# Performance work log

Measured on AMD Instinct MI355X. Metric: run time of the kernel, lower is better.

The kernel has to match this reference:

```python
import jax, jax.numpy as jnp
import numpy as np

B, S, H = 2, 8192, 1024
NUM_HEADS = 16
HEAD_DIM = H // NUM_HEADS
KERNEL = 7
DILATION = 1
SCALE = 1.0 / np.sqrt(HEAD_DIM)


def setup_inputs() -> dict:
    key = jax.random.key(0)
    ks = jax.random.split(key, 9)
    init = 0.02
    return {
        "hidden_states": jax.random.normal(ks[0], (B, S, H), dtype=jnp.float32),
        "w_q": jax.random.normal(ks[1], (H, H), dtype=jnp.float32) * init,
        "b_q": jnp.zeros((H,), dtype=jnp.float32),
        "w_k": jax.random.normal(ks[2], (H, H), dtype=jnp.float32) * init,
        "b_k": jnp.zeros((H,), dtype=jnp.float32),
        "w_v": jax.random.normal(ks[3], (H, H), dtype=jnp.float32) * init,
        "b_v": jnp.zeros((H,), dtype=jnp.float32),
        "w_o": jax.random.normal(ks[4], (H, H), dtype=jnp.float32) * init,
        "b_o": jnp.zeros((H,), dtype=jnp.float32),
    }


def reference(hidden_states, w_q, b_q, w_k, b_k, w_v, b_v, w_o, b_o):
    b, s, h = hidden_states.shape
    # QKV projections (weights stored [in, out])
    q = hidden_states @ w_q + b_q
    k = hidden_states @ w_k + b_k
    v = hidden_states @ w_v + b_v
    # [B, nH, S, hd]
    q = q.reshape(b, s, NUM_HEADS, HEAD_DIM).transpose(0, 2, 1, 3)
    k = k.reshape(b, s, NUM_HEADS, HEAD_DIM).transpose(0, 2, 1, 3)
    v = v.reshape(b, s, NUM_HEADS, HEAD_DIM).transpose(0, 2, 1, 3)

    # Neighborhood window indices: for query i, keys at i + (j - K//2)*dilation
    offsets = (jnp.arange(KERNEL) - KERNEL // 2) * DILATION  # [K]
    idx = jnp.arange(s)[:, None] + offsets[None, :]          # [S, K]
    valid = (idx >= 0) & (idx < s)                           # [S, K]
    idx_c = jnp.clip(idx, 0, s - 1)

    k_win = k[:, :, idx_c, :]  # [B, nH, S, K, hd]
    v_win = v[:, :, idx_c, :]  # [B, nH, S, K, hd]

    scores = jnp.einsum('bhsd,bhskd->bhsk', q, k_win) * SCALE
    scores = jnp.where(valid[None, None], scores, -jnp.inf)
    attn = jax.nn.softmax(scores, axis=-1)                   # [B, nH, S, K]
    out = jnp.einsum('bhsk,bhskd->bhsd', attn, v_win)        # [B, nH, S, hd]

    out = out.transpose(0, 2, 1, 3).reshape(b, s, h)
    return out @ w_o + b_o
```

## Files before the change

### kernel.cpp

```cpp
#include <hip/hip_runtime.h>


typedef __bf16 bf16x8 __attribute__((ext_vector_type(8)));
typedef float f32x4 __attribute__((ext_vector_type(4)));
typedef int int4v __attribute__((ext_vector_type(4)));
typedef __attribute__((address_space(1))) void as1_void;
typedef __attribute__((address_space(3))) void as3_void;

__device__ __forceinline__ float bf2f(unsigned short u) {
    union { unsigned int u; float f; } c;
    c.u = ((unsigned int)u) << 16;
    return c.f;
}
__device__ __forceinline__ unsigned short f2bf(float f) {
    union { float f; unsigned int u; } c;
    c.f = f;
    unsigned int u = c.u;
    u += 0x7fffu + ((u >> 16) & 1u);
    return (unsigned short)(u >> 16);
}

__global__ __launch_bounds__(256) void cast_kernel(
    const float* __restrict__ in, unsigned short* __restrict__ out, int n4) {
    int i = blockIdx.x * 256 + threadIdx.x;
    if (i < n4) {
        float4 v = ((const float4*)in)[i];
        ushort4 o;
        o.x = f2bf(v.x); o.y = f2bf(v.y); o.z = f2bf(v.z); o.w = f2bf(v.w);
        ((ushort4*)out)[i] = o;
    }
}

__global__ __launch_bounds__(256) void transpose_cast(
    const float* __restrict__ W, unsigned short* __restrict__ Wt) {
    __shared__ unsigned short tile[32][33];
    const int c0 = blockIdx.x * 32;
    const int r0 = blockIdx.y * 32;
    const int tx = threadIdx.x;
    const int ty = threadIdx.y;
#pragma unroll
    for (int i = 0; i < 32; i += 8)
        tile[ty + i][tx] = f2bf(W[(size_t)(r0 + ty + i) * 1024 + c0 + tx]);
    __syncthreads();
#pragma unroll
    for (int i = 0; i < 32; i += 8)
        Wt[(size_t)(c0 + ty + i) * 1024 + r0 + tx] = tile[tx][ty + i];
}

__global__ __launch_bounds__(256) void concat_bias(
    const float* __restrict__ a, const float* __restrict__ b,
    const float* __restrict__ c, float* __restrict__ o) {
    int i = blockIdx.x * 256 + threadIdx.x;
    if (i < 3072)
        o[i] = (i < 1024) ? a[i] : ((i < 2048) ? b[i - 1024] : c[i - 2048]);
}

template <int MODE>
__global__ __launch_bounds__(256) void gemm_bt(
    const unsigned short* __restrict__ A, const unsigned short* __restrict__ Bt,
    const float* __restrict__ bias, float* __restrict__ Cf,
    unsigned short* __restrict__ Cb, unsigned short* __restrict__ Vt,
    int N, int K) {
    __shared__ unsigned short smem[16384];
    const int tid = threadIdx.x;
    const int lane = tid & 63;
    const int wave = tid >> 6;
    const int bm = blockIdx.y * 128;
    const int bn = blockIdx.x * 128;
    const int wm = (wave >> 1) * 64;
    const int wn = (wave & 1) * 64;
    const int quad = lane >> 4;
    const int mr = lane & 15;

    const unsigned short* gA[4];
    const unsigned short* gB[4];
    char* lA[4];
    char* lB[4];
#pragma unroll
    for (int k = 0; k < 4; ++k) {
        const int q = (k * 4 + wave) * 64 + lane;
        const int row = q >> 3;
        const int c8 = (q & 7) ^ (row & 7);
        gA[k] = A + (size_t)(bm + row) * K + c8 * 8;
        gB[k] = Bt + (size_t)(bn + row) * K + c8 * 8;
        lA[k] = (char*)smem + (size_t)(k * 4 + wave) * 1024;
        lB[k] = (char*)smem + 16384 + (size_t)(k * 4 + wave) * 1024;
    }

    f32x4 acc[4][4] = {};

    for (int kt = 0; kt < K; kt += 64) {
#pragma unroll
        for (int k = 0; k < 4; ++k) {
            __builtin_amdgcn_global_load_lds((as1_void*)gA[k], (as3_void*)lA[k], 16, 0, 0);
            __builtin_amdgcn_global_load_lds((as1_void*)gB[k], (as3_void*)lB[k], 16, 0, 0);
            gA[k] += 64; gB[k] += 64;
        }
        __syncthreads();

#pragma unroll
        for (int kk = 0; kk < 2; ++kk) {
            bf16x8 af[4], bfr[4];
#pragma unroll
            for (int i = 0; i < 4; ++i) {
                const int R = wm + i * 16 + mr;
                const int c8 = (kk * 4 + quad) ^ (mr & 7);
                af[i] = *(const bf16x8*)(smem + R * 64 + c8 * 8);
            }
#pragma unroll
            for (int j = 0; j < 4; ++j) {
                const int R = wn + j * 16 + mr;
                const int c8 = (kk * 4 + quad) ^ (mr & 7);
                bfr[j] = *(const bf16x8*)(smem + 8192 + R * 64 + c8 * 8);
            }
#pragma unroll
            for (int i = 0; i < 4; ++i)
#pragma unroll
                for (int j = 0; j < 4; ++j)
                    acc[i][j] = __builtin_amdgcn_mfma_f32_16x16x32_bf16(
                        af[i], bfr[j], acc[i][j], 0, 0, 0);
        }
        __syncthreads();
    }

    if (MODE == 0 || bn < 2048) {
#pragma unroll
        for (int j = 0; j < 4; ++j) {
            const int gcol = bn + wn + j * 16 + mr;
            const float bv = bias[gcol];
#pragma unroll
            for (int i = 0; i < 4; ++i) {
                const int gr = bm + wm + i * 16 + quad * 4;
#pragma unroll
                for (int r = 0; r < 4; ++r) {
                    const float v = acc[i][j][r] + bv;
                    if (MODE == 0) Cf[(size_t)(gr + r) * N + gcol] = v;
                    else           Cb[(size_t)(gr + r) * 2048 + gcol] = f2bf(v);
                }
            }
        }
    } else {
        unsigned short* ep = smem + wave * 2048;
        const int bb = (bm + wm) >> 13;
        const int ssb = (bm + wm) & 8191;
        const int lr = ((lane & 15) == lane ? 0 : 0);
#pragma unroll
        for (int j = 0; j < 4; ++j) {
            const int gcol = bn + wn + j * 16 + mr;
            const float bv = bias[gcol];
#pragma unroll
            for (int i = 0; i < 4; ++i)
#pragma unroll
                for (int r = 0; r < 4; ++r)
                    ep[mr * 68 + i * 16 + quad * 4 + r] = f2bf(acc[i][j][r] + bv);
            const size_t vrow0 = (size_t)(bb * 1024 + (bn - 2048) + wn + j * 16);
#pragma unroll
            for (int p = 0; p < 4; ++p) {
                const int dr = (p * 64 + lane) >> 4;
                const int ch = lane & 15;
                uint2 val = *(const uint2*)(ep + dr * 68 + ch * 4);
                *(uint2*)(Vt + (vrow0 + dr) * 8192 + ssb + ch * 4) = val;
            }
        }
        (void)lr;
    }
}

__global__ __launch_bounds__(256) void attn_mfma(
    const unsigned short* __restrict__ QK, const unsigned short* __restrict__ Vt,
    unsigned short* __restrict__ out) {
    __shared__ unsigned short sP[4][64 * 104];
    const int tid = threadIdx.x;
    const int lane = tid & 63;
    const int wave = tid >> 6;
    const int quad = lane >> 4;
    const int cc = lane & 15;
    const int w = blockIdx.x * 4 + wave;
    const int b = w >> 11;
    const int h = (w >> 7) & 15;
    const int st = w & 127;
    const int s0 = st << 6;
    const int win0 = s0 - 8;
    const size_t tokBase = (size_t)b * 8192;
    unsigned short* P = sP[wave];

    {
        int4v z = {0, 0, 0, 0};
#pragma unroll
        for (int i = 0; i < 13; ++i)
            *(int4v*)(P + i * 512 + lane * 8) = z;
    }

    f32x4 accS[4][5] = {};
#pragma unroll
    for (int kc = 0; kc < 2; ++kc) {
        bf16x8 qf[4], kf[5];
#pragma unroll
        for (int mt = 0; mt < 4; ++mt)
            qf[mt] = *(const bf16x8*)(QK + (tokBase + s0 + mt * 16 + cc) * 2048
                                      + h * 64 + kc * 32 + quad * 8);
#pragma unroll
        for (int nt = 0; nt < 5; ++nt) {
            int row = win0 + nt * 16 + cc;
            row = row < 0 ? 0 : (row > 8191 ? 8191 : row);
            kf[nt] = *(const bf16x8*)(QK + (tokBase + row) * 2048
                                      + 1024 + h * 64 + kc * 32 + quad * 8);
        }
#pragma unroll
        for (int mt = 0; mt < 4; ++mt)
#pragma unroll
            for (int nt = 0; nt < 5; ++nt)
                accS[mt][nt] = __builtin_amdgcn_mfma_f32_16x16x32_bf16(
                    qf[mt], kf[nt], accS[mt][nt], 0, 0, 0);
    }

    const float NEG = -__builtin_inff();
#pragma unroll
    for (int mt = 0; mt < 4; ++mt) {
#pragma unroll
        for (int r = 0; r < 4; ++r) {
            const int mrow = mt * 16 + quad * 4 + r;
            float v[5];
#pragma unroll
            for (int nt = 0; nt < 5; ++nt) {
                const int k = nt * 16 + cc;
                const int rel = k - mrow;
                const int sidx = win0 + k;
                const bool ok = (rel >= 5) & (rel <= 11) & (sidx >= 0) & (sidx < 8192);
                v[nt] = ok ? accS[mt][nt][r] * 0.125f : NEG;
            }
            float mx = v[0];
#pragma unroll
            for (int nt = 1; nt < 5; ++nt) mx = fmaxf(mx, v[nt]);
#pragma unroll
            for (int off = 8; off >= 1; off >>= 1) mx = fmaxf(mx, __shfl_xor(mx, off));
            float p[5], sum = 0.f;
#pragma unroll
            for (int nt = 0; nt < 5; ++nt) {
                p[nt] = __builtin_amdgcn_exp2f((v[nt] - mx) * 1.44269504f);
                sum += p[nt];
            }
#pragma unroll
            for (int off = 8; off >= 1; off >>= 1) sum += __shfl_xor(sum, off);
            const float inv = __builtin_amdgcn_rcpf(sum);
#pragma unroll
            for (int nt = 0; nt < 5; ++nt)
                P[mrow * 104 + nt * 16 + cc] = f2bf(p[nt] * inv);
        }
    }

    f32x4 accO[4][4] = {};
#pragma unroll
    for (int kc = 0; kc < 3; ++kc) {
        bf16x8 pf[4], vf[4];
#pragma unroll
        for (int mt = 0; mt < 4; ++mt)
            pf[mt] = *(const bf16x8*)(P + (mt * 16 + cc) * 104 + kc * 32 + quad * 8);
        {
            int pos = win0 + kc * 32 + quad * 8;
            pos = pos < 0 ? 0 : (pos > 8184 ? 8184 : pos);
#pragma unroll
            for (int nt = 0; nt < 4; ++nt)
                vf[nt] = *(const bf16x8*)(Vt + ((size_t)(b * 16 + h) * 64 + nt * 16 + cc) * 8192 + pos);
        }
#pragma unroll
        for (int mt = 0; mt < 4; ++mt)
#pragma unroll
            for (int nt = 0; nt < 4; ++nt)
                accO[mt][nt] = __builtin_amdgcn_mfma_f32_16x16x32_bf16(
                    pf[mt], vf[nt], accO[mt][nt], 0, 0, 0);
    }

#pragma unroll
    for (int mt = 0; mt < 4; ++mt)
#pragma unroll
        for (int nt = 0; nt < 4; ++nt)
#pragma unroll
            for (int r = 0; r < 4; ++r)
                P[(mt * 16 + quad * 4 + r) * 72 + nt * 16 + cc] = f2bf(accO[mt][nt][r]);

#pragma unroll
    for (int pass = 0; pass < 8; ++pass) {
        const int row = pass * 8 + (lane >> 3);
        const int ch = lane & 7;
        int4v vv = *(const int4v*)(P + row * 72 + ch * 8);
        *(int4v*)(out + (tokBase + s0 + row) * 1024 + h * 64 + ch * 8) = vv;
    }
}

extern "C" void kernel_launch(void* const* d_in, const int* in_sizes, int n_in,
                              void* d_out, int out_size, void* d_ws, size_t ws_size,
                              hipStream_t stream) {
    (void)in_sizes; (void)n_in; (void)out_size; (void)ws_size;
    const float* X  = (const float*)d_in[0];
    const float* wq = (const float*)d_in[1];
    const float* bq = (const float*)d_in[2];
    const float* wk = (const float*)d_in[3];
    const float* bk = (const float*)d_in[4];
    const float* wv = (const float*)d_in[5];
    const float* bv = (const float*)d_in[6];
    const float* wo = (const float*)d_in[7];
    const float* bo = (const float*)d_in[8];
    float* out = (float*)d_out;

    char* ws = (char*)d_ws;
    unsigned short* Xb    = (unsigned short*)(ws);
    unsigned short* WtQKV = (unsigned short*)(ws + 33554432);
    unsigned short* WtO   = (unsigned short*)(ws + 39845888);
    unsigned short* QK    = (unsigned short*)(ws + 41943040);
    unsigned short* Vt    = (unsigned short*)(ws + 109051904);
    unsigned short* AttnO = (unsigned short*)(ws + 142606336);
    float*          biasQ = (float*)(ws + 176160768);

    cast_kernel<<<16384, 256, 0, stream>>>(X, Xb, 4194304);

    dim3 tb(32, 8), tg(32, 32);
    transpose_cast<<<tg, tb, 0, stream>>>(wq, WtQKV);
    transpose_cast<<<tg, tb, 0, stream>>>(wk, WtQKV + 1024 * 1024);
    transpose_cast<<<tg, tb, 0, stream>>>(wv, WtQKV + 2 * 1024 * 1024);
    transpose_cast<<<tg, tb, 0, stream>>>(wo, WtO);
    concat_bias<<<12, 256, 0, stream>>>(bq, bk, bv, biasQ);

    gemm_bt<1><<<dim3(24, 128), 256, 0, stream>>>(Xb, WtQKV, biasQ, nullptr, QK, Vt, 3072, 1024);

    attn_mfma<<<1024, 256, 0, stream>>>(QK, Vt, AttnO);

    gemm_bt<0><<<dim3(8, 128), 256, 0, stream>>>(AttnO, WtO, bo, out, nullptr, nullptr, 1024, 1024);
}
```

Before: 353.9 us.

## Stage GEMM epilogues through LDS, swizzle tile order, merge weight transposes

The GEMM epilogues now stage each wave's output tile in shared memory and write rows back with 16-byte vector stores, replacing scattered scalar stores for both the fp32 output and the bf16 Q/K outputs. Block indices are remapped so groups of 16 row-tiles sweep across the columns together, which is meant to improve L2 reuse of the A and B operands. The four weight transpose-cast launches are merged into one launch over a z dimension, cutting launch overhead. The extra LDS round trip adds a little shared-memory traffic and instruction work in the epilogue.

```diff
diff --git a/kernel.cpp b/kernel.cpp
--- a/kernel.cpp
+++ b/kernel.cpp
@@ -31,13 +31,18 @@
     }
 }
 
-__global__ __launch_bounds__(256) void transpose_cast(
-    const float* __restrict__ W, unsigned short* __restrict__ Wt) {
+__global__ __launch_bounds__(256) void transpose_cast4(
+    const float* __restrict__ w0, const float* __restrict__ w1,
+    const float* __restrict__ w2, const float* __restrict__ w3,
+    unsigned short* __restrict__ t0, unsigned short* __restrict__ t3) {
     __shared__ unsigned short tile[32][33];
+    const int z = blockIdx.z;
+    const float* W = (z == 0) ? w0 : (z == 1) ? w1 : (z == 2) ? w2 : w3;
+    unsigned short* Wt = (z == 3) ? t3 : t0 + (size_t)z * 1048576;
     const int c0 = blockIdx.x * 32;
     const int r0 = blockIdx.y * 32;
-    const int tx = threadIdx.x;
-    const int ty = threadIdx.y;
+    const int tx = threadIdx.x & 31;
+    const int ty = threadIdx.x >> 5;
 #pragma unroll
     for (int i = 0; i < 32; i += 8)
         tile[ty + i][tx] = f2bf(W[(size_t)(r0 + ty + i) * 1024 + c0 + tx]);
@@ -56,7 +61,7 @@
 }
 
 template <int MODE>
-__global__ __launch_bounds__(256) void gemm_bt(
+__device__ __forceinline__ void gemm_body(
     const unsigned short* __restrict__ A, const unsigned short* __restrict__ Bt,
     const float* __restrict__ bias, float* __restrict__ Cf,
     unsigned short* __restrict__ Cb, unsigned short* __restrict__ Vt,
@@ -65,8 +70,15 @@
     const int tid = threadIdx.x;
     const int lane = tid & 63;
     const int wave = tid >> 6;
-    const int bm = blockIdx.y * 128;
-    const int bn = blockIdx.x * 128;
+
+    const int nbx = gridDim.x;
+    const int n = blockIdx.y * nbx + blockIdx.x;
+    const int per = nbx * 16;
+    const int g = n / per;
+    const int rm = n - g * per;
+    const int bm = (g * 16 + (rm & 15)) * 128;
+    const int bn = (rm >> 4) * 128;
+
     const int wm = (wave >> 1) * 64;
     const int wn = (wave & 1) * 64;
     const int quad = lane >> 4;
@@ -123,27 +135,48 @@
         __syncthreads();
     }
 
-    if (MODE == 0 || bn < 2048) {
+    if (MODE == 0) {
+        float* epf = (float*)smem + wave * 2048;
 #pragma unroll
         for (int j = 0; j < 4; ++j) {
-            const int gcol = bn + wn + j * 16 + mr;
-            const float bv = bias[gcol];
-#pragma unroll
-            for (int i = 0; i < 4; ++i) {
-                const int gr = bm + wm + i * 16 + quad * 4;
-#pragma unroll
-                for (int r = 0; r < 4; ++r) {
-                    const float v = acc[i][j][r] + bv;
-                    if (MODE == 0) Cf[(size_t)(gr + r) * N + gcol] = v;
-                    else           Cb[(size_t)(gr + r) * 2048 + gcol] = f2bf(v);
-                }
+            const int gcol0 = bn + wn + j * 16;
+            const float bv = bias[gcol0 + mr];
+#pragma unroll
+            for (int i = 0; i < 4; ++i)
+#pragma unroll
+                for (int r = 0; r < 4; ++r)
+                    epf[(i * 16 + quad * 4 + r) * 20 + mr] = acc[i][j][r] + bv;
+#pragma unroll
+            for (int p = 0; p < 4; ++p) {
+                const int dr = p * 16 + (lane >> 2);
+                const int ch = lane & 3;
+                f32x4 v = *(const f32x4*)(epf + dr * 20 + ch * 4);
+                *(f32x4*)(Cf + (size_t)(bm + wm + dr) * N + gcol0 + ch * 4) = v;
+            }
+        }
+    } else if (bn < 2048) {
+        unsigned short* epb = smem + wave * 4096;
+#pragma unroll
+        for (int j = 0; j < 4; ++j) {
+            const int gcol0 = bn + wn + j * 16;
+            const float bv = bias[gcol0 + mr];
+#pragma unroll
+            for (int i = 0; i < 4; ++i)
+#pragma unroll
+                for (int r = 0; r < 4; ++r)
+                    epb[(i * 16 + quad * 4 + r) * 20 + mr] = f2bf(acc[i][j][r] + bv);
+#pragma unroll
+            for (int p = 0; p < 2; ++p) {
+                const int dr = p * 32 + (lane >> 1);
+                const int ch = lane & 1;
+                int4v v = *(const int4v*)(epb + dr * 20 + ch * 8);
+                *(int4v*)(Cb + (size_t)(bm + wm + dr) * 2048 + gcol0 + ch * 8) = v;
             }
         }
     } else {
-        unsigned short* ep = smem + wave * 2048;
+        unsigned short* ep = smem + wave * 4096;
         const int bb = (bm + wm) >> 13;
         const int ssb = (bm + wm) & 8191;
-        const int lr = ((lane & 15) == lane ? 0 : 0);
 #pragma unroll
         for (int j = 0; j < 4; ++j) {
             const int gcol = bn + wn + j * 16 + mr;
@@ -162,8 +195,20 @@
                 *(uint2*)(Vt + (vrow0 + dr) * 8192 + ssb + ch * 4) = val;
             }
         }
-        (void)lr;
-    }
+    }
+}
+
+__global__ __launch_bounds__(256) void gemm_qkv(
+    const unsigned short* __restrict__ A, const unsigned short* __restrict__ Bt,
+    const float* __restrict__ bias, unsigned short* __restrict__ Cb,
+    unsigned short* __restrict__ Vt, int N, int K) {
+    gemm_body<1>(A, Bt, bias, nullptr, Cb, Vt, N, K);
+}
+
+__global__ __launch_bounds__(256) void gemm_out(
+    const unsigned short* __restrict__ A, const unsigned short* __restrict__ Bt,
+    const float* __restrict__ bias, float* __restrict__ Cf, int N, int K) {
+    gemm_body<0>(A, Bt, bias, Cf, nullptr, nullptr, N, K);
 }
 
 __global__ __launch_bounds__(256) void attn_mfma(
@@ -313,17 +358,12 @@
     float*          biasQ = (float*)(ws + 176160768);
 
     cast_kernel<<<16384, 256, 0, stream>>>(X, Xb, 4194304);
-
-    dim3 tb(32, 8), tg(32, 32);
-    transpose_cast<<<tg, tb, 0, stream>>>(wq, WtQKV);
-    transpose_cast<<<tg, tb, 0, stream>>>(wk, WtQKV + 1024 * 1024);
-    transpose_cast<<<tg, tb, 0, stream>>>(wv, WtQKV + 2 * 1024 * 1024);
-    transpose_cast<<<tg, tb, 0, stream>>>(wo, WtO);
+    transpose_cast4<<<dim3(32, 32, 4), 256, 0, stream>>>(wq, wk, wv, wo, WtQKV, WtO);
     concat_bias<<<12, 256, 0, stream>>>(bq, bk, bv, biasQ);
 
-    gemm_bt<1><<<dim3(24, 128), 256, 0, stream>>>(Xb, WtQKV, biasQ, nullptr, QK, Vt, 3072, 1024);
+    gemm_qkv<<<dim3(24, 128), 256, 0, stream>>>(Xb, WtQKV, biasQ, QK, Vt, 3072, 1024);
 
     attn_mfma<<<1024, 256, 0, stream>>>(QK, Vt, AttnO);
 
-    gemm_bt<0><<<dim3(8, 128), 256, 0, stream>>>(AttnO, WtO, bo, out, nullptr, nullptr, 1024, 1024);
-}
+    gemm_out<<<dim3(8, 128), 256, 0, stream>>>(AttnO, WtO, bo, out, 1024, 1024);
+}
```

Result: no change. 354.6 us (+0.2%).
